# Kernel tuning notes

Measured on AMD Instinct MI355X. Metric: run time of the kernel, lower is better.

## Reference

```python
import jax, jax.numpy as jnp
import numpy as np

DIM = 192
HID = 128
EPS = 1e-8
ITERS = 3
LN_EPS = 1e-5
SCALE = DIM ** (-0.5)


def layer_norm(x, w, b):
    mu = x.mean(axis=-1, keepdims=True)
    var = ((x - mu) ** 2).mean(axis=-1, keepdims=True)
    return (x - mu) * jax.lax.rsqrt(var + LN_EPS) * w + b


def gru_cell(x, h, Wih, Whh, bih, bhh):
    # PyTorch GRUCell: gates ordered (r, z, n)
    gx = x @ Wih.T + bih          # [M, 3*DIM]
    gh = h @ Whh.T + bhh          # [M, 3*DIM]
    xr, xz, xn = jnp.split(gx, 3, axis=-1)
    hr, hz, hn = jnp.split(gh, 3, axis=-1)
    r = jax.nn.sigmoid(xr + hr)
    z = jax.nn.sigmoid(xz + hz)
    n = jnp.tanh(xn + r * hn)
    return (1.0 - z) * n + z * h


def setup_inputs() -> dict:
    key = jax.random.key(0)
    ks = jax.random.split(key, 12)
    B, N, K = 64, 4096, 11
    s = 0.02
    return {
        "inputs": jax.random.normal(ks[0], (B, N, DIM), jnp.float32),
        "noise": jax.random.normal(ks[1], (B, K, DIM), jnp.float32),
        "slots_mu": jax.random.normal(ks[2], (1, 1, DIM), jnp.float32),
        "slots_sigma": jax.random.uniform(ks[3], (1, 1, DIM), jnp.float32),
        "ln_in_w": jnp.ones((DIM,), jnp.float32),
        "ln_in_b": jnp.zeros((DIM,), jnp.float32),
        "ln_slots_w": jnp.ones((DIM,), jnp.float32),
        "ln_slots_b": jnp.zeros((DIM,), jnp.float32),
        "ln_mlp_w": jnp.ones((DIM,), jnp.float32),
        "ln_mlp_b": jnp.zeros((DIM,), jnp.float32),
        "Wq": jax.random.normal(ks[4], (DIM, DIM), jnp.float32) * s,
        "bq": jnp.zeros((DIM,), jnp.float32),
        "Wk": jax.random.normal(ks[5], (DIM, DIM), jnp.float32) * s,
        "bk": jnp.zeros((DIM,), jnp.float32),
        "Wv": jax.random.normal(ks[6], (DIM, DIM), jnp.float32) * s,
        "bv": jnp.zeros((DIM,), jnp.float32),
        "gru_Wih": jax.random.normal(ks[7], (3 * DIM, DIM), jnp.float32) * s,
        "gru_Whh": jax.random.normal(ks[8], (3 * DIM, DIM), jnp.float32) * s,
        "gru_bih": jnp.zeros((3 * DIM,), jnp.float32),
        "gru_bhh": jnp.zeros((3 * DIM,), jnp.float32),
        "mlp_W1": jax.random.normal(ks[9], (DIM, HID), jnp.float32) * s,
        "mlp_b1": jnp.zeros((HID,), jnp.float32),
        "mlp_W2": jax.random.normal(ks[10], (HID, DIM), jnp.float32) * s,
        "mlp_b2": jnp.zeros((DIM,), jnp.float32),
        "n_slots": 11,
    }


def reference(inputs, noise, slots_mu, slots_sigma,
              ln_in_w, ln_in_b, ln_slots_w, ln_slots_b, ln_mlp_w, ln_mlp_b,
              Wq, bq, Wk, bk, Wv, bv,
              gru_Wih, gru_Whh, gru_bih, gru_bhh,
              mlp_W1, mlp_b1, mlp_W2, mlp_b2, n_slots):
    B, N, _ = inputs.shape
    # slots ~ Normal(mu, sigma), reparameterized with fixed noise
    slots = slots_mu + slots_sigma * noise            # [B, K, D]
    x = layer_norm(inputs, ln_in_w, ln_in_b)
    key_vec = x @ Wk + bk                             # [B, N, D]
    val_vec = x @ Wv + bv                             # [B, N, D]
    attn_output = None
    for _ in range(ITERS):
        slots_prev = slots
        s_n = layer_norm(slots, ln_slots_w, ln_slots_b)
        q = s_n @ Wq + bq                             # [B, K, D]
        dots = jnp.einsum('bkd,bnd->bkn', q, key_vec) * SCALE
        attn = jax.nn.softmax(dots, axis=1) + EPS     # softmax over slots axis
        attn_output = attn
        attn = attn / attn.sum(axis=-1, keepdims=True)
        updates = jnp.einsum('bnd,bkn->bkd', val_vec, attn)
        h = gru_cell(updates.reshape(-1, DIM), slots_prev.reshape(-1, DIM),
                     gru_Wih, gru_Whh, gru_bih, gru_bhh)
        slots = h.reshape(B, -1, DIM)
        m = layer_norm(slots, ln_mlp_w, ln_mlp_b)
        m = jax.nn.relu(m @ mlp_W1 + mlp_b1) @ mlp_W2 + mlp_b2
        slots = slots + m
    return (slots, attn_output)
```

## Files before the change

kernel.cpp:

```cpp
#include <hip/hip_runtime.h>
#include <hip/hip_bf16.h>
#include <cstdint>
#include <cstddef>

#define DIM 192
#define NSL 11
#define NB 64
#define NN 4096
#define HIDN 128
#define NCHP 16
#define TROWS 32
#define NT 8
#define LN_EPS 1e-5f
#define EPS_A 1e-8f
#define SCALE_Q 0.07216878364870323f

__device__ __forceinline__ float wred(float v) {
#pragma unroll
  for (int m = 32; m; m >>= 1) v += __shfl_xor(v, m, 64);
  return v;
}

typedef const __attribute__((address_space(1))) void gas_void;
typedef __attribute__((address_space(3))) void las_void;
__device__ __forceinline__ void gload_lds16(const void* g, void* l) {
  __builtin_amdgcn_global_load_lds((gas_void*)g, (las_void*)l, 16, 0, 0);
}

__global__ __launch_bounds__(256) void k_tr(
    const float* __restrict__ Wih, const float* __restrict__ Whh, const float* __restrict__ Wk,
    float* __restrict__ WihT, float* __restrict__ WhhT, float* __restrict__ WkT) {
  __shared__ float t[64][65];
  int tile = blockIdx.x;
  const float* src; float* dst; int R, C;
  if (tile < 27)      { src = Wih; dst = WihT; R = 576; C = 192; }
  else if (tile < 54) { src = Whh; dst = WhhT; R = 576; C = 192; tile -= 27; }
  else                { src = Wk;  dst = WkT;  R = 192; C = 192; tile -= 54; }
  const int ntc = C >> 6;
  const int tr = tile / ntc, tc = tile % ntc;
  const int lane = threadIdx.x & 63, w = threadIdx.x >> 6;
#pragma unroll
  for (int i = 0; i < 16; ++i) {
    int row = w * 16 + i;
    t[row][lane] = src[(size_t)(tr * 64 + row) * C + tc * 64 + lane];
  }
  __syncthreads();
#pragma unroll
  for (int i = 0; i < 16; ++i) {
    int row = w * 16 + i;
    dst[(size_t)(tc * 64 + row) * R + tr * 64 + lane] = t[lane][row];
  }
}

__global__ __launch_bounds__(192) void k_prep(
    const float* __restrict__ lnw, const float* __restrict__ lnb,
    const float* __restrict__ Wq, const float* __restrict__ bq,
    const float* __restrict__ WkT, const float* __restrict__ bk,
    const float* __restrict__ xw, const float* __restrict__ xb,
    const float* __restrict__ noise, const float* __restrict__ mu0, const float* __restrict__ sig,
    float* __restrict__ slots_ws,
    float* __restrict__ qt, float* __restrict__ t0g, float* __restrict__ cpg) {
  const int b = blockIdx.x, kg = blockIdx.y, tid = threadIdx.x;
  const int k0 = kg * 3, kcnt = (kg == 3) ? 2 : 3;
  const int wave = tid >> 6, lane = tid & 63;
  const int j = tid;
  __shared__ __align__(16) float sn[3][DIM];
  __shared__ __align__(16) float qb[3][DIM];
  __shared__ float red[3][3][2];

#pragma unroll
  for (int kk = 0; kk < 3; ++kk) {
    if (kk < kcnt) {
      float v = mu0[j] + sig[j] * noise[(size_t)(b * NSL + k0 + kk) * DIM + j];
      sn[kk][j] = v;
      slots_ws[(size_t)(b * NSL + k0 + kk) * DIM + j] = v;
    } else sn[kk][j] = 0.f;
  }
  __syncthreads();

  for (int kk = wave; kk < 3; kk += 3) {
    float a = sn[kk][lane], c = sn[kk][lane + 64], e = sn[kk][lane + 128];
    float s = wred(a + c + e), ss = wred(a * a + c * c + e * e);
    float mu = s * (1.0f / DIM), var = ss * (1.0f / DIM) - mu * mu;
    float rstd = rsqrtf(var + LN_EPS);
    sn[kk][lane]       = (a - mu) * rstd * lnw[lane]       + lnb[lane];
    sn[kk][lane + 64]  = (c - mu) * rstd * lnw[lane + 64]  + lnb[lane + 64];
    sn[kk][lane + 128] = (e - mu) * rstd * lnw[lane + 128] + lnb[lane + 128];
  }
  __syncthreads();

  float acc[3];
  const float bj = bq[j];
#pragma unroll
  for (int kk = 0; kk < 3; ++kk) acc[kk] = bj;
  for (int d = 0; d < DIM; d += 4) {
    float w0 = Wq[(d + 0) * DIM + j], w1 = Wq[(d + 1) * DIM + j];
    float w2 = Wq[(d + 2) * DIM + j], w3 = Wq[(d + 3) * DIM + j];
#pragma unroll
    for (int kk = 0; kk < 3; ++kk) {
      float4 s4 = *(const float4*)&sn[kk][d];
      acc[kk] = fmaf(s4.w, w3, fmaf(s4.z, w2, fmaf(s4.y, w1, fmaf(s4.x, w0, acc[kk]))));
    }
  }
#pragma unroll
  for (int kk = 0; kk < 3; ++kk) qb[kk][j] = acc[kk];
  __syncthreads();

  float qk[3];
#pragma unroll
  for (int kk = 0; kk < 3; ++kk) qk[kk] = 0.f;
  for (int d = 0; d < DIM; d += 4) {
    float w0 = WkT[(d + 0) * DIM + j], w1 = WkT[(d + 1) * DIM + j];
    float w2 = WkT[(d + 2) * DIM + j], w3 = WkT[(d + 3) * DIM + j];
#pragma unroll
    for (int kk = 0; kk < 3; ++kk) {
      float4 q4 = *(const float4*)&qb[kk][d];
      qk[kk] = fmaf(q4.w, w3, fmaf(q4.z, w2, fmaf(q4.y, w1, fmaf(q4.x, w0, qk[kk]))));
    }
  }
  const float wj = xw[j], bxj = xb[j], bkj = bk[j];
#pragma unroll
  for (int kk = 0; kk < 3; ++kk) {
    float qtv = SCALE_Q * wj * qk[kk];
    if (kk < kcnt) qt[(size_t)(b * NSL + k0 + kk) * DIM + j] = qtv;
    float r1 = wred(qtv);
    float r2 = wred(SCALE_Q * (bxj * qk[kk] + qb[kk][j] * bkj));
    if (lane == 0) { red[wave][kk][0] = r1; red[wave][kk][1] = r2; }
  }
  __syncthreads();
  if (tid < kcnt) {
    t0g[b * NSL + k0 + tid] = red[0][tid][0] + red[1][tid][0] + red[2][tid][0];
    cpg[b * NSL + k0 + tid] = red[0][tid][1] + red[1][tid][1] + red[2][tid][1];
  }
}

__global__ __launch_bounds__(256) void k_iter(
    const float* __restrict__ x, const float* __restrict__ qt,
    const float* __restrict__ t0g, const float* __restrict__ cpg,
    float* __restrict__ attn_out, float* __restrict__ P1p,
    float* __restrict__ S_p, float* __restrict__ m1_p) {
  __shared__ __align__(16) float xs[2][TROWS * DIM];
  __shared__ __align__(16) float qs[NSL * DIM];
  __shared__ __align__(16) float a_lds[TROWS][12];
  __shared__ float rs_lds[TROWS];
  __shared__ float t0s[NSL], cps[NSL];
  __shared__ float redS[4][NSL], redM[4][NSL];

  const int b = blockIdx.x, ch = blockIdx.y, tid = threadIdx.x;
  const int lane = tid & 63, wv = tid >> 6;
  const int widx = tid & 15, g = tid >> 4;

  const float* xbase = x + ((size_t)b * NN + ch * 256) * DIM;

  {
#pragma unroll
    for (int i = 0; i < 6; ++i) {
      int c = i * 4 + wv;
      gload_lds16(xbase + c * 256 + lane * 4, &xs[0][c * 256]);
    }
  }
  {
    const float4* src = (const float4*)(qt + (size_t)b * NSL * DIM);
    float4* dst = (float4*)qs;
    dst[tid] = src[tid];
    dst[256 + tid] = src[256 + tid];
    if (tid < 16) dst[512 + tid] = src[512 + tid];
  }
  if (tid < NSL) { t0s[tid] = t0g[b * NSL + tid]; cps[tid] = cpg[b * NSL + tid]; }

  float acc[3][NSL], sS[NSL], sM[NSL];
#pragma unroll
  for (int k = 0; k < NSL; ++k) {
    acc[0][k] = 0.f; acc[1][k] = 0.f; acc[2][k] = 0.f;
    sS[k] = 0.f; sM[k] = 0.f;
  }

#pragma unroll 1
  for (int T = 0; T < NT; ++T) {
    const int cur = T & 1;
    __syncthreads();
    if (T < NT - 1) {
      const float* src = xbase + (size_t)(T + 1) * TROWS * DIM;
      float* dstb = &xs[cur ^ 1][0];
#pragma unroll
      for (int i = 0; i < 6; ++i) {
        int c = i * 4 + wv;
        gload_lds16(src + c * 256 + lane * 4, dstb + c * 256);
      }
      asm volatile("s_waitcnt vmcnt(6)" ::: "memory");
    } else {
      asm volatile("s_waitcnt vmcnt(0)" ::: "memory");
    }
    __builtin_amdgcn_s_barrier();
    const float* xc = &xs[cur][0];

    float dot[2][NSL], st_s[2], st_ss[2];
#pragma unroll
    for (int rr = 0; rr < 2; ++rr) {
      st_s[rr] = 0.f; st_ss[rr] = 0.f;
#pragma unroll
      for (int k = 0; k < NSL; ++k) dot[rr][k] = 0.f;
    }
#pragma unroll
    for (int w = 0; w < 3; ++w) {
      const int c4 = widx + 16 * w;
      float4 xr[2];
#pragma unroll
      for (int rr = 0; rr < 2; ++rr) {
        xr[rr] = ((const float4*)xc)[(2 * g + rr) * 48 + c4];
        st_s[rr] += (xr[rr].x + xr[rr].y) + (xr[rr].z + xr[rr].w);
        st_ss[rr] = fmaf(xr[rr].x, xr[rr].x, fmaf(xr[rr].y, xr[rr].y,
                    fmaf(xr[rr].z, xr[rr].z, fmaf(xr[rr].w, xr[rr].w, st_ss[rr]))));
      }
#pragma unroll
      for (int k = 0; k < NSL; ++k) {
        float4 qv = *(const float4*)&qs[k * DIM + 4 * c4];
#pragma unroll
        for (int rr = 0; rr < 2; ++rr)
          dot[rr][k] = fmaf(xr[rr].w, qv.w, fmaf(xr[rr].z, qv.z,
                       fmaf(xr[rr].y, qv.y, fmaf(xr[rr].x, qv.x, dot[rr][k]))));
      }
    }
#pragma unroll
    for (int m = 1; m <= 8; m <<= 1) {
#pragma unroll
      for (int rr = 0; rr < 2; ++rr) {
        st_s[rr] += __shfl_xor(st_s[rr], m, 64);
        st_ss[rr] += __shfl_xor(st_ss[rr], m, 64);
#pragma unroll
        for (int k = 0; k < NSL; ++k) dot[rr][k] += __shfl_xor(dot[rr][k], m, 64);
      }
    }
    if ((widx & 7) == 0) {
      const int hi = widx >> 3;
      const int r = 2 * g + hi;
      float dsel[NSL];
#pragma unroll
      for (int k = 0; k < NSL; ++k) dsel[k] = (widx == 0) ? dot[0][k] : dot[1][k];
      float sts  = (widx == 0) ? st_s[0]  : st_s[1];
      float stss = (widx == 0) ? st_ss[0] : st_ss[1];
      float mu = sts * (1.0f / DIM);
      float var = stss * (1.0f / DIM) - mu * mu;
      float rstd = rsqrtf(var + LN_EPS);
      float murstd = mu * rstd;
      float dv[NSL];
#pragma unroll
      for (int k = 0; k < NSL; ++k) dv[k] = fmaf(rstd, dsel[k], fmaf(-murstd, t0s[k], cps[k]));
      float mx = dv[0];
#pragma unroll
      for (int k = 1; k < NSL; ++k) mx = fmaxf(mx, dv[k]);
      float es[NSL], sum = 0.f;
#pragma unroll
      for (int k = 0; k < NSL; ++k) { es[k] = __expf(dv[k] - mx); sum += es[k]; }
      float inv = 1.0f / sum;
#pragma unroll
      for (int k = 0; k < NSL; ++k) {
        float a = fmaf(es[k], inv, EPS_A);
        a_lds[r][k] = a;
        sS[k] += a;
        sM[k] = fmaf(a, murstd, sM[k]);
      }
      rs_lds[r] = rstd;
    }
    asm volatile("s_waitcnt lgkmcnt(0)" ::: "memory");
    __builtin_amdgcn_s_barrier();

    {
      int idx = tid;
      attn_out[((size_t)(b * NSL + (idx >> 5))) * NN + ch * 256 + T * TROWS + (idx & 31)]
          = a_lds[idx & 31][idx >> 5];
      idx = tid + 256;
      if (idx < NSL * TROWS)
        attn_out[((size_t)(b * NSL + (idx >> 5))) * NN + ch * 256 + T * TROWS + (idx & 31)]
            = a_lds[idx & 31][idx >> 5];
    }
#pragma unroll 4
    for (int i = 0; i < 8; ++i) {
      const int r = 4 * i + wv;
      float rst = rs_lds[r];
      float4 a0 = *(const float4*)&a_lds[r][0];
      float4 a1 = *(const float4*)&a_lds[r][4];
      float4 a2 = *(const float4*)&a_lds[r][8];
#pragma unroll
      for (int j = 0; j < 3; ++j) {
        const int col = lane + 64 * j;
        float t1 = rst * xc[r * DIM + col];
        acc[j][0]  = fmaf(a0.x, t1, acc[j][0]);
        acc[j][1]  = fmaf(a0.y, t1, acc[j][1]);
        acc[j][2]  = fmaf(a0.z, t1, acc[j][2]);
        acc[j][3]  = fmaf(a0.w, t1, acc[j][3]);
        acc[j][4]  = fmaf(a1.x, t1, acc[j][4]);
        acc[j][5]  = fmaf(a1.y, t1, acc[j][5]);
        acc[j][6]  = fmaf(a1.z, t1, acc[j][6]);
        acc[j][7]  = fmaf(a1.w, t1, acc[j][7]);
        acc[j][8]  = fmaf(a2.x, t1, acc[j][8]);
        acc[j][9]  = fmaf(a2.y, t1, acc[j][9]);
        acc[j][10] = fmaf(a2.z, t1, acc[j][10]);
      }
    }
  }

  __syncthreads();
  float* accbuf = &xs[0][0];
#pragma unroll
  for (int j = 0; j < 3; ++j)
#pragma unroll
    for (int k = 0; k < NSL; ++k)
      accbuf[tid * 33 + j * 11 + k] = acc[j][k];
  __syncthreads();
  if (tid < DIM) {
    const int l = tid & 63, j = tid >> 6;
#pragma unroll
    for (int k = 0; k < NSL; ++k) {
      float v = accbuf[(l) * 33 + j * 11 + k] + accbuf[(64 + l) * 33 + j * 11 + k]
              + accbuf[(128 + l) * 33 + j * 11 + k] + accbuf[(192 + l) * 33 + j * 11 + k];
      P1p[(((size_t)b * NCHP + ch) * NSL + k) * DIM + tid] = v;
    }
  }
#pragma unroll
  for (int k = 0; k < NSL; ++k) { sS[k] = wred(sS[k]); sM[k] = wred(sM[k]); }
  if (lane == 0) {
#pragma unroll
    for (int k = 0; k < NSL; ++k) { redS[wv][k] = sS[k]; redM[wv][k] = sM[k]; }
  }
  __syncthreads();
  if (tid < NSL) {
    S_p[((size_t)b * NCHP + ch) * NSL + tid]  = redS[0][tid] + redS[1][tid] + redS[2][tid] + redS[3][tid];
    m1_p[((size_t)b * NCHP + ch) * NSL + tid] = redM[0][tid] + redM[1][tid] + redM[2][tid] + redM[3][tid];
  }
}

__global__ __launch_bounds__(192) void k_step(
    const float* __restrict__ P1p, const float* __restrict__ m1_p, const float* __restrict__ S_p,
    const float* __restrict__ xw, const float* __restrict__ xb,
    const float* __restrict__ Wv, const float* __restrict__ bv,
    const float* __restrict__ slots_in,
    const float* __restrict__ WihT, const float* __restrict__ WhhT,
    const float* __restrict__ bih, const float* __restrict__ bhh,
    const float* __restrict__ mw, const float* __restrict__ mb,
    const float* __restrict__ W1, const float* __restrict__ b1,
    const float* __restrict__ W2, const float* __restrict__ b2,
    const float* __restrict__ sw, const float* __restrict__ sb,
    const float* __restrict__ Wq, const float* __restrict__ bq,
    const float* __restrict__ WkT, const float* __restrict__ bk,
    float* __restrict__ slots_ws, float* __restrict__ slots_out,
    float* __restrict__ qt, float* __restrict__ t0g, float* __restrict__ cpg) {
  const int b = blockIdx.x, kg = blockIdx.y, tid = threadIdx.x;
  const int k0 = kg * 3, kcnt = (kg == 3) ? 2 : 3;
  const int wave = tid >> 6, lane = tid & 63;
  const int j = tid;
  __shared__ __align__(16) float u[3][DIM];
  __shared__ __align__(16) float hp[3][DIM];
  __shared__ __align__(16) float h[3][DIM];
  __shared__ __align__(16) float hid[3][HIDN];
  __shared__ float red[3][3][2];

  const float wj = xw[j], bj = xb[j];
#pragma unroll
  for (int kk = 0; kk < 3; ++kk) {
    if (kk < kcnt) {
      float p = 0.f, S = 0.f, M = 0.f;
#pragma unroll
      for (int ch = 0; ch < NCHP; ++ch) {
        p += P1p[(((size_t)b * NCHP + ch) * NSL + k0 + kk) * DIM + j];
        S += S_p[((size_t)b * NCHP + ch) * NSL + k0 + kk];
        M += m1_p[((size_t)b * NCHP + ch) * NSL + k0 + kk];
      }
      float inv = 1.0f / S;
      u[kk][j]  = wj * (p - M) * inv + bj;
      hp[kk][j] = slots_in[(size_t)(b * NSL + k0 + kk) * DIM + j];
    } else { u[kk][j] = 0.f; hp[kk][j] = 0.f; }
  }
  __syncthreads();

  float upd[3];
  const float bvj = bv[j];
#pragma unroll
  for (int kk = 0; kk < 3; ++kk) upd[kk] = bvj;
  for (int d = 0; d < DIM; d += 4) {
    float w0 = Wv[(d + 0) * DIM + j], w1 = Wv[(d + 1) * DIM + j];
    float w2 = Wv[(d + 2) * DIM + j], w3 = Wv[(d + 3) * DIM + j];
#pragma unroll
    for (int kk = 0; kk < 3; ++kk) {
      float4 x4 = *(const float4*)&u[kk][d];
      upd[kk] = fmaf(x4.w, w3, fmaf(x4.z, w2, fmaf(x4.y, w1, fmaf(x4.x, w0, upd[kk]))));
    }
  }
  __syncthreads();
#pragma unroll
  for (int kk = 0; kk < 3; ++kk) u[kk][j] = upd[kk];
  __syncthreads();

  float xr[3], xz[3], xn[3], hr[3], hz[3], hn[3];
  {
    float br_ = bih[j], bz_ = bih[DIM + j], bn_ = bih[2 * DIM + j];
    float cr_ = bhh[j], cz_ = bhh[DIM + j], cn_ = bhh[2 * DIM + j];
#pragma unroll
    for (int kk = 0; kk < 3; ++kk) { xr[kk] = br_; xz[kk] = bz_; xn[kk] = bn_; hr[kk] = cr_; hz[kk] = cz_; hn[kk] = cn_; }
  }
  for (int d = 0; d < DIM; d += 2) {
#pragma unroll
    for (int dd = 0; dd < 2; ++dd) {
      const float* ihrow = WihT + (size_t)(d + dd) * 576;
      const float* hhrow = WhhT + (size_t)(d + dd) * 576;
      float ar = ihrow[j], az = ihrow[192 + j], an = ihrow[384 + j];
      float br = hhrow[j], bz = hhrow[192 + j], bn = hhrow[384 + j];
#pragma unroll
      for (int kk = 0; kk < 3; ++kk) {
        float uv = u[kk][d + dd];
        float pv = hp[kk][d + dd];
        xr[kk] = fmaf(uv, ar, xr[kk]);
        xz[kk] = fmaf(uv, az, xz[kk]);
        xn[kk] = fmaf(uv, an, xn[kk]);
        hr[kk] = fmaf(pv, br, hr[kk]);
        hz[kk] = fmaf(pv, bz, hz[kk]);
        hn[kk] = fmaf(pv, bn, hn[kk]);
      }
    }
  }
#pragma unroll
  for (int kk = 0; kk < 3; ++kk) {
    float r = 1.f / (1.f + __expf(-(xr[kk] + hr[kk])));
    float z = 1.f / (1.f + __expf(-(xz[kk] + hz[kk])));
    float n = tanhf(xn[kk] + r * hn[kk]);
    h[kk][j] = (1.f - z) * n + z * hp[kk][j];
  }
  __syncthreads();

  for (int kk = wave; kk < 3; kk += 3) {
    float a = h[kk][lane], c = h[kk][lane + 64], e = h[kk][lane + 128];
    float s = wred(a + c + e), ss = wred(a * a + c * c + e * e);
    float mu = s * (1.0f / DIM), var = ss * (1.0f / DIM) - mu * mu;
    float rstd = rsqrtf(var + LN_EPS);
    u[kk][lane]       = (a - mu) * rstd * mw[lane]       + mb[lane];
    u[kk][lane + 64]  = (c - mu) * rstd * mw[lane + 64]  + mb[lane + 64];
    u[kk][lane + 128] = (e - mu) * rstd * mw[lane + 128] + mb[lane + 128];
  }
  __syncthreads();

  for (int t = tid; t < kcnt * HIDN; t += 192) {
    int kk = t >> 7, c = t & (HIDN - 1);
    float acc = b1[c];
    for (int d = 0; d < DIM; d += 4) {
      float4 m4 = *(const float4*)&u[kk][d];
      acc = fmaf(m4.x, W1[(d + 0) * HIDN + c],
            fmaf(m4.y, W1[(d + 1) * HIDN + c],
            fmaf(m4.z, W1[(d + 2) * HIDN + c],
            fmaf(m4.w, W1[(d + 3) * HIDN + c], acc))));
    }
    hid[kk][c] = fmaxf(acc, 0.f);
  }
  __syncthreads();

#pragma unroll 1
  for (int kk = 0; kk < kcnt; ++kk) {
    float acc = b2[j];
    for (int c = 0; c < HIDN; c += 4) {
      float4 h4 = *(const float4*)&hid[kk][c];
      acc = fmaf(h4.x, W2[(c + 0) * DIM + j],
            fmaf(h4.y, W2[(c + 1) * DIM + j],
            fmaf(h4.z, W2[(c + 2) * DIM + j],
            fmaf(h4.w, W2[(c + 3) * DIM + j], acc))));
    }
    float outv = h[kk][j] + acc;
    size_t gi = (size_t)(b * NSL + k0 + kk) * DIM + j;
    slots_ws[gi] = outv;
    slots_out[gi] = outv;
    hp[kk][j] = outv;
  }
  __syncthreads();

  for (int kk = wave; kk < 3; kk += 3) {
    float a = hp[kk][lane], c = hp[kk][lane + 64], e = hp[kk][lane + 128];
    float s = wred(a + c + e), ss = wred(a * a + c * c + e * e);
    float mu = s * (1.0f / DIM), var = ss * (1.0f / DIM) - mu * mu;
    float rstd = rsqrtf(var + LN_EPS);
    u[kk][lane]       = (a - mu) * rstd * sw[lane]       + sb[lane];
    u[kk][lane + 64]  = (c - mu) * rstd * sw[lane + 64]  + sb[lane + 64];
    u[kk][lane + 128] = (e - mu) * rstd * sw[lane + 128] + sb[lane + 128];
  }
  __syncthreads();

  float qacc[3];
  const float bqj = bq[j];
#pragma unroll
  for (int kk = 0; kk < 3; ++kk) qacc[kk] = bqj;
  for (int d = 0; d < DIM; d += 4) {
    float w0 = Wq[(d + 0) * DIM + j], w1 = Wq[(d + 1) * DIM + j];
    float w2 = Wq[(d + 2) * DIM + j], w3 = Wq[(d + 3) * DIM + j];
#pragma unroll
    for (int kk = 0; kk < 3; ++kk) {
      float4 s4 = *(const float4*)&u[kk][d];
      qacc[kk] = fmaf(s4.w, w3, fmaf(s4.z, w2, fmaf(s4.y, w1, fmaf(s4.x, w0, qacc[kk]))));
    }
  }
  __syncthreads();
#pragma unroll
  for (int kk = 0; kk < 3; ++kk) h[kk][j] = qacc[kk];
  __syncthreads();

  float qk[3];
#pragma unroll
  for (int kk = 0; kk < 3; ++kk) qk[kk] = 0.f;
  for (int d = 0; d < DIM; d += 4) {
    float w0 = WkT[(d + 0) * DIM + j], w1 = WkT[(d + 1) * DIM + j];
    float w2 = WkT[(d + 2) * DIM + j], w3 = WkT[(d + 3) * DIM + j];
#pragma unroll
    for (int kk = 0; kk < 3; ++kk) {
      float4 q4 = *(const float4*)&h[kk][d];
      qk[kk] = fmaf(q4.w, w3, fmaf(q4.z, w2, fmaf(q4.y, w1, fmaf(q4.x, w0, qk[kk]))));
    }
  }
  const float wxj = xw[j], bxj = xb[j], bkj = bk[j];
#pragma unroll
  for (int kk = 0; kk < 3; ++kk) {
    float qtv = SCALE_Q * wxj * qk[kk];
    if (kk < kcnt) qt[(size_t)(b * NSL + k0 + kk) * DIM + j] = qtv;
    float r1 = wred(qtv);
    float r2 = wred(SCALE_Q * (bxj * qk[kk] + h[kk][j] * bkj));
    if (lane == 0) { red[wave][kk][0] = r1; red[wave][kk][1] = r2; }
  }
  __syncthreads();
  if (tid < kcnt) {
    t0g[b * NSL + k0 + tid] = red[0][tid][0] + red[1][tid][0] + red[2][tid][0];
    cpg[b * NSL + k0 + tid] = red[0][tid][1] + red[1][tid][1] + red[2][tid][1];
  }
}

extern "C" void kernel_launch(void* const* d_in, const int* in_sizes, int n_in,
                              void* d_out, int out_size, void* d_ws, size_t ws_size,
                              hipStream_t stream) {
  const float* inputs      = (const float*)d_in[0];
  const float* noise       = (const float*)d_in[1];
  const float* slots_mu    = (const float*)d_in[2];
  const float* slots_sigma = (const float*)d_in[3];
  const float* ln_in_w     = (const float*)d_in[4];
  const float* ln_in_b     = (const float*)d_in[5];
  const float* ln_slots_w  = (const float*)d_in[6];
  const float* ln_slots_b  = (const float*)d_in[7];
  const float* ln_mlp_w    = (const float*)d_in[8];
  const float* ln_mlp_b    = (const float*)d_in[9];
  const float* Wq  = (const float*)d_in[10];
  const float* bq  = (const float*)d_in[11];
  const float* Wk  = (const float*)d_in[12];
  const float* bk  = (const float*)d_in[13];
  const float* Wv  = (const float*)d_in[14];
  const float* bv  = (const float*)d_in[15];
  const float* Wih = (const float*)d_in[16];
  const float* Whh = (const float*)d_in[17];
  const float* bih = (const float*)d_in[18];
  const float* bhh = (const float*)d_in[19];
  const float* W1  = (const float*)d_in[20];
  const float* b1  = (const float*)d_in[21];
  const float* W2  = (const float*)d_in[22];
  const float* b2  = (const float*)d_in[23];

  float* out = (float*)d_out;
  float* slots_out = out;
  float* attn_out  = out + NB * NSL * DIM;

  char* w = (char*)d_ws;
  float* slots = (float*)w;
  float* qt    = (float*)(w + 540672);
  float* t0g   = (float*)(w + 1081344);
  float* cpg   = (float*)(w + 1084160);
  float* P1p   = (float*)(w + 1086976);
  float* S_p   = (float*)(w + 9737728);
  float* m1_p  = (float*)(w + 9782784);
  float* WihT  = (float*)(w + 9827840);
  float* WhhT  = (float*)(w + 10270208);
  float* WkT   = (float*)(w + 10712576);

  k_tr<<<63, 256, 0, stream>>>(Wih, Whh, Wk, WihT, WhhT, WkT);
  k_prep<<<dim3(NB, 4), 192, 0, stream>>>(ln_slots_w, ln_slots_b, Wq, bq, WkT, bk,
                                          ln_in_w, ln_in_b, noise, slots_mu, slots_sigma,
                                          slots, qt, t0g, cpg);
  for (int it = 0; it < 3; ++it) {
    k_iter<<<dim3(NB, NCHP), 256, 0, stream>>>(inputs, qt, t0g, cpg, attn_out, P1p, S_p, m1_p);
    k_step<<<dim3(NB, 4), 192, 0, stream>>>(P1p, m1_p, S_p, ln_in_w, ln_in_b, Wv, bv, slots,
                                            WihT, WhhT, bih, bhh, ln_mlp_w, ln_mlp_b,
                                            W1, b1, W2, b2, ln_slots_w, ln_slots_b,
                                            Wq, bq, WkT, bk, slots, slots_out, qt, t0g, cpg);
  }
}
```

Measured before the change: 771.8 us.

## Single-buffer x tile in k_iter for occupancy; one slot per k_step block

k_iter drops its double-buffered LDS tile for a single buffer and requests 4 blocks per CU through launch bounds, so each tile load is now waited on before compute. The cross-wave accumulator reduction is done in two passes so it fits in the smaller buffer. k_step now handles one slot per block (grid NB x 11) instead of three, giving more blocks with fewer registers each. The aim is higher occupancy and parallelism, at the cost of losing load/compute overlap within a block and re-reading weights per slot.

```diff
diff --git a/kernel.cpp b/kernel.cpp
--- a/kernel.cpp
+++ b/kernel.cpp
@@ -134,12 +134,12 @@
   }
 }
 
-__global__ __launch_bounds__(256) void k_iter(
+__global__ __launch_bounds__(256, 4) void k_iter(
     const float* __restrict__ x, const float* __restrict__ qt,
     const float* __restrict__ t0g, const float* __restrict__ cpg,
     float* __restrict__ attn_out, float* __restrict__ P1p,
     float* __restrict__ S_p, float* __restrict__ m1_p) {
-  __shared__ __align__(16) float xs[2][TROWS * DIM];
+  __shared__ __align__(16) float xs[TROWS * DIM];
   __shared__ __align__(16) float qs[NSL * DIM];
   __shared__ __align__(16) float a_lds[TROWS][12];
   __shared__ float rs_lds[TROWS];
@@ -152,12 +152,10 @@
 
   const float* xbase = x + ((size_t)b * NN + ch * 256) * DIM;
 
-  {
-#pragma unroll
-    for (int i = 0; i < 6; ++i) {
-      int c = i * 4 + wv;
-      gload_lds16(xbase + c * 256 + lane * 4, &xs[0][c * 256]);
-    }
+#pragma unroll
+  for (int i = 0; i < 6; ++i) {
+    int c = i * 4 + wv;
+    gload_lds16(xbase + c * 256 + lane * 4, &xs[c * 256]);
   }
   {
     const float4* src = (const float4*)(qt + (size_t)b * NSL * DIM);
@@ -177,22 +175,19 @@
 
 #pragma unroll 1
   for (int T = 0; T < NT; ++T) {
-    const int cur = T & 1;
-    __syncthreads();
-    if (T < NT - 1) {
-      const float* src = xbase + (size_t)(T + 1) * TROWS * DIM;
-      float* dstb = &xs[cur ^ 1][0];
+    if (T == 0) {
+      __syncthreads();
+    } else {
+      __syncthreads();
+      const float* src = xbase + (size_t)T * TROWS * DIM;
 #pragma unroll
       for (int i = 0; i < 6; ++i) {
         int c = i * 4 + wv;
-        gload_lds16(src + c * 256 + lane * 4, dstb + c * 256);
+        gload_lds16(src + c * 256 + lane * 4, &xs[c * 256]);
       }
-      asm volatile("s_waitcnt vmcnt(6)" ::: "memory");
-    } else {
       asm volatile("s_waitcnt vmcnt(0)" ::: "memory");
-    }
-    __builtin_amdgcn_s_barrier();
-    const float* xc = &xs[cur][0];
+      __builtin_amdgcn_s_barrier();
+    }
 
     float dot[2][NSL], st_s[2], st_ss[2];
 #pragma unroll
@@ -207,7 +202,7 @@
       float4 xr[2];
 #pragma unroll
       for (int rr = 0; rr < 2; ++rr) {
-        xr[rr] = ((const float4*)xc)[(2 * g + rr) * 48 + c4];
+        xr[rr] = ((const float4*)xs)[(2 * g + rr) * 48 + c4];
         st_s[rr] += (xr[rr].x + xr[rr].y) + (xr[rr].z + xr[rr].w);
         st_ss[rr] = fmaf(xr[rr].x, xr[rr].x, fmaf(xr[rr].y, xr[rr].y,
                     fmaf(xr[rr].z, xr[rr].z, fmaf(xr[rr].w, xr[rr].w, st_ss[rr]))));
@@ -284,7 +279,7 @@
 #pragma unroll
       for (int j = 0; j < 3; ++j) {
         const int col = lane + 64 * j;
-        float t1 = rst * xc[r * DIM + col];
+        float t1 = rst * xs[r * DIM + col];
         acc[j][0]  = fmaf(a0.x, t1, acc[j][0]);
         acc[j][1]  = fmaf(a0.y, t1, acc[j][1]);
         acc[j][2]  = fmaf(a0.z, t1, acc[j][2]);
@@ -301,19 +296,29 @@
   }
 
   __syncthreads();
-  float* accbuf = &xs[0][0];
-#pragma unroll
-  for (int j = 0; j < 3; ++j)
-#pragma unroll
-    for (int k = 0; k < NSL; ++k)
-      accbuf[tid * 33 + j * 11 + k] = acc[j][k];
+  float* accbuf = &xs[0];
+  const int slot = tid & 127;
+  if (wv < 2) {
+#pragma unroll
+    for (int j = 0; j < 3; ++j)
+#pragma unroll
+      for (int k = 0; k < NSL; ++k)
+        accbuf[slot * 33 + j * 11 + k] = acc[j][k];
+  }
+  __syncthreads();
+  if (wv >= 2) {
+#pragma unroll
+    for (int j = 0; j < 3; ++j)
+#pragma unroll
+      for (int k = 0; k < NSL; ++k)
+        accbuf[slot * 33 + j * 11 + k] += acc[j][k];
+  }
   __syncthreads();
   if (tid < DIM) {
     const int l = tid & 63, j = tid >> 6;
 #pragma unroll
     for (int k = 0; k < NSL; ++k) {
-      float v = accbuf[(l) * 33 + j * 11 + k] + accbuf[(64 + l) * 33 + j * 11 + k]
-              + accbuf[(128 + l) * 33 + j * 11 + k] + accbuf[(192 + l) * 33 + j * 11 + k];
+      float v = accbuf[l * 33 + j * 11 + k] + accbuf[(64 + l) * 33 + j * 11 + k];
       P1p[(((size_t)b * NCHP + ch) * NSL + k) * DIM + tid] = v;
     }
   }
@@ -345,185 +350,160 @@
     const float* __restrict__ WkT, const float* __restrict__ bk,
     float* __restrict__ slots_ws, float* __restrict__ slots_out,
     float* __restrict__ qt, float* __restrict__ t0g, float* __restrict__ cpg) {
-  const int b = blockIdx.x, kg = blockIdx.y, tid = threadIdx.x;
-  const int k0 = kg * 3, kcnt = (kg == 3) ? 2 : 3;
+  const int b = blockIdx.x, k = blockIdx.y, tid = threadIdx.x;
   const int wave = tid >> 6, lane = tid & 63;
   const int j = tid;
-  __shared__ __align__(16) float u[3][DIM];
-  __shared__ __align__(16) float hp[3][DIM];
-  __shared__ __align__(16) float h[3][DIM];
-  __shared__ __align__(16) float hid[3][HIDN];
-  __shared__ float red[3][3][2];
-
-  const float wj = xw[j], bj = xb[j];
-#pragma unroll
-  for (int kk = 0; kk < 3; ++kk) {
-    if (kk < kcnt) {
-      float p = 0.f, S = 0.f, M = 0.f;
-#pragma unroll
-      for (int ch = 0; ch < NCHP; ++ch) {
-        p += P1p[(((size_t)b * NCHP + ch) * NSL + k0 + kk) * DIM + j];
-        S += S_p[((size_t)b * NCHP + ch) * NSL + k0 + kk];
-        M += m1_p[((size_t)b * NCHP + ch) * NSL + k0 + kk];
-      }
-      float inv = 1.0f / S;
-      u[kk][j]  = wj * (p - M) * inv + bj;
-      hp[kk][j] = slots_in[(size_t)(b * NSL + k0 + kk) * DIM + j];
-    } else { u[kk][j] = 0.f; hp[kk][j] = 0.f; }
-  }
-  __syncthreads();
-
-  float upd[3];
-  const float bvj = bv[j];
-#pragma unroll
-  for (int kk = 0; kk < 3; ++kk) upd[kk] = bvj;
+  __shared__ __align__(16) float u[DIM];
+  __shared__ __align__(16) float hp[DIM];
+  __shared__ __align__(16) float h[DIM];
+  __shared__ __align__(16) float hid[HIDN];
+  __shared__ float red[3][2];
+
+  {
+    float p = 0.f, S = 0.f, M = 0.f;
+#pragma unroll
+    for (int ch = 0; ch < NCHP; ++ch) {
+      p += P1p[(((size_t)b * NCHP + ch) * NSL + k) * DIM + j];
+      S += S_p[((size_t)b * NCHP + ch) * NSL + k];
+      M += m1_p[((size_t)b * NCHP + ch) * NSL + k];
+    }
+    float inv = 1.0f / S;
+    u[j]  = xw[j] * (p - M) * inv + xb[j];
+    hp[j] = slots_in[(size_t)(b * NSL + k) * DIM + j];
+  }
+  __syncthreads();
+
+  float upd = bv[j];
+#pragma unroll 2
   for (int d = 0; d < DIM; d += 4) {
-    float w0 = Wv[(d + 0) * DIM + j], w1 = Wv[(d + 1) * DIM + j];
-    float w2 = Wv[(d + 2) * DIM + j], w3 = Wv[(d + 3) * DIM + j];
-#pragma unroll
-    for (int kk = 0; kk < 3; ++kk) {
-      float4 x4 = *(const float4*)&u[kk][d];
-      upd[kk] = fmaf(x4.w, w3, fmaf(x4.z, w2, fmaf(x4.y, w1, fmaf(x4.x, w0, upd[kk]))));
-    }
-  }
-  __syncthreads();
-#pragma unroll
-  for (int kk = 0; kk < 3; ++kk) u[kk][j] = upd[kk];
-  __syncthreads();
-
-  float xr[3], xz[3], xn[3], hr[3], hz[3], hn[3];
-  {
-    float br_ = bih[j], bz_ = bih[DIM + j], bn_ = bih[2 * DIM + j];
-    float cr_ = bhh[j], cz_ = bhh[DIM + j], cn_ = bhh[2 * DIM + j];
-#pragma unroll
-    for (int kk = 0; kk < 3; ++kk) { xr[kk] = br_; xz[kk] = bz_; xn[kk] = bn_; hr[kk] = cr_; hz[kk] = cz_; hn[kk] = cn_; }
-  }
-  for (int d = 0; d < DIM; d += 2) {
-#pragma unroll
-    for (int dd = 0; dd < 2; ++dd) {
+    float4 u4 = *(const float4*)&u[d];
+    upd = fmaf(u4.x, Wv[(d + 0) * DIM + j],
+          fmaf(u4.y, Wv[(d + 1) * DIM + j],
+          fmaf(u4.z, Wv[(d + 2) * DIM + j],
+          fmaf(u4.w, Wv[(d + 3) * DIM + j], upd))));
+  }
+  __syncthreads();
+  u[j] = upd;
+  __syncthreads();
+
+  float xr = bih[j], xz = bih[DIM + j], xn = bih[2 * DIM + j];
+  float hr = bhh[j], hz = bhh[DIM + j], hn = bhh[2 * DIM + j];
+#pragma unroll 2
+  for (int d = 0; d < DIM; d += 4) {
+    float4 u4 = *(const float4*)&u[d];
+    float4 p4 = *(const float4*)&hp[d];
+    float us[4] = {u4.x, u4.y, u4.z, u4.w};
+    float ps[4] = {p4.x, p4.y, p4.z, p4.w};
+#pragma unroll
+    for (int dd = 0; dd < 4; ++dd) {
       const float* ihrow = WihT + (size_t)(d + dd) * 576;
       const float* hhrow = WhhT + (size_t)(d + dd) * 576;
-      float ar = ihrow[j], az = ihrow[192 + j], an = ihrow[384 + j];
-      float br = hhrow[j], bz = hhrow[192 + j], bn = hhrow[384 + j];
-#pragma unroll
-      for (int kk = 0; kk < 3; ++kk) {
-        float uv = u[kk][d + dd];
-        float pv = hp[kk][d + dd];
-        xr[kk] = fmaf(uv, ar, xr[kk]);
-        xz[kk] = fmaf(uv, az, xz[kk]);
-        xn[kk] = fmaf(uv, an, xn[kk]);
-        hr[kk] = fmaf(pv, br, hr[kk]);
-        hz[kk] = fmaf(pv, bz, hz[kk]);
-        hn[kk] = fmaf(pv, bn, hn[kk]);
-      }
-    }
-  }
-#pragma unroll
-  for (int kk = 0; kk < 3; ++kk) {
-    float r = 1.f / (1.f + __expf(-(xr[kk] + hr[kk])));
-    float z = 1.f / (1.f + __expf(-(xz[kk] + hz[kk])));
-    float n = tanhf(xn[kk] + r * hn[kk]);
-    h[kk][j] = (1.f - z) * n + z * hp[kk][j];
-  }
-  __syncthreads();
-
-  for (int kk = wave; kk < 3; kk += 3) {
-    float a = h[kk][lane], c = h[kk][lane + 64], e = h[kk][lane + 128];
+      xr = fmaf(us[dd], ihrow[j], xr);
+      xz = fmaf(us[dd], ihrow[192 + j], xz);
+      xn = fmaf(us[dd], ihrow[384 + j], xn);
+      hr = fmaf(ps[dd], hhrow[j], hr);
+      hz = fmaf(ps[dd], hhrow[192 + j], hz);
+      hn = fmaf(ps[dd], hhrow[384 + j], hn);
+    }
+  }
+  float hv;
+  {
+    float r = 1.f / (1.f + __expf(-(xr + hr)));
+    float z = 1.f / (1.f + __expf(-(xz + hz)));
+    float n = tanhf(xn + r * hn);
+    hv = (1.f - z) * n + z * hp[j];
+    h[j] = hv;
+  }
+  __syncthreads();
+
+  {
+    float a = h[lane], c = h[lane + 64], e = h[lane + 128];
     float s = wred(a + c + e), ss = wred(a * a + c * c + e * e);
     float mu = s * (1.0f / DIM), var = ss * (1.0f / DIM) - mu * mu;
     float rstd = rsqrtf(var + LN_EPS);
-    u[kk][lane]       = (a - mu) * rstd * mw[lane]       + mb[lane];
-    u[kk][lane + 64]  = (c - mu) * rstd * mw[lane + 64]  + mb[lane + 64];
-    u[kk][lane + 128] = (e - mu) * rstd * mw[lane + 128] + mb[lane + 128];
-  }
-  __syncthreads();
-
-  for (int t = tid; t < kcnt * HIDN; t += 192) {
-    int kk = t >> 7, c = t & (HIDN - 1);
-    float acc = b1[c];
+    u[lane]       = (a - mu) * rstd * mw[lane]       + mb[lane];
+    u[lane + 64]  = (c - mu) * rstd * mw[lane + 64]  + mb[lane + 64];
+    u[lane + 128] = (e - mu) * rstd * mw[lane + 128] + mb[lane + 128];
+  }
+  __syncthreads();
+
+  if (tid < HIDN) {
+    float acc = b1[tid];
+#pragma unroll 2
     for (int d = 0; d < DIM; d += 4) {
-      float4 m4 = *(const float4*)&u[kk][d];
-      acc = fmaf(m4.x, W1[(d + 0) * HIDN + c],
-            fmaf(m4.y, W1[(d + 1) * HIDN + c],
-            fmaf(m4.z, W1[(d + 2) * HIDN + c],
-            fmaf(m4.w, W1[(d + 3) * HIDN + c], acc))));
-    }
-    hid[kk][c] = fmaxf(acc, 0.f);
-  }
-  __syncthreads();
-
-#pragma unroll 1
-  for (int kk = 0; kk < kcnt; ++kk) {
+      float4 m4 = *(const float4*)&u[d];
+      acc = fmaf(m4.x, W1[(d + 0) * HIDN + tid],
+            fmaf(m4.y, W1[(d + 1) * HIDN + tid],
+            fmaf(m4.z, W1[(d + 2) * HIDN + tid],
+            fmaf(m4.w, W1[(d + 3) * HIDN + tid], acc))));
+    }
+    hid[tid] = fmaxf(acc, 0.f);
+  }
+  __syncthreads();
+
+  float outv;
+  {
     float acc = b2[j];
+#pragma unroll 2
     for (int c = 0; c < HIDN; c += 4) {
-      float4 h4 = *(const float4*)&hid[kk][c];
+      float4 h4 = *(const float4*)&hid[c];
       acc = fmaf(h4.x, W2[(c + 0) * DIM + j],
             fmaf(h4.y, W2[(c + 1) * DIM + j],
             fmaf(h4.z, W2[(c + 2) * DIM + j],
             fmaf(h4.w, W2[(c + 3) * DIM + j], acc))));
     }
-    float outv = h[kk][j] + acc;
-    size_t gi = (size_t)(b * NSL + k0 + kk) * DIM + j;
+    outv = hv + acc;
+    size_t gi = (size_t)(b * NSL + k) * DIM + j;
     slots_ws[gi] = outv;
     slots_out[gi] = outv;
-    hp[kk][j] = outv;
-  }
-  __syncthreads();
-
-  for (int kk = wave; kk < 3; kk += 3) {
-    float a = hp[kk][lane], c = hp[kk][lane + 64], e = hp[kk][lane + 128];
+    hp[j] = outv;
+  }
+  __syncthreads();
+
+  {
+    float a = hp[lane], c = hp[lane + 64], e = hp[lane + 128];
     float s = wred(a + c + e), ss = wred(a * a + c * c + e * e);
     float mu = s * (1.0f / DIM), var = ss * (1.0f / DIM) - mu * mu;
     float rstd = rsqrtf(var + LN_EPS);
-    u[kk][lane]       = (a - mu) * rstd * sw[lane]       + sb[lane];
-    u[kk][lane + 64]  = (c - mu) * rstd * sw[lane + 64]  + sb[lane + 64];
-    u[kk][lane + 128] = (e - mu) * rstd * sw[lane + 128] + sb[lane + 128];
-  }
-  __syncthreads();
-
-  float qacc[3];
-  const float bqj = bq[j];
-#pragma unroll
-  for (int kk = 0; kk < 3; ++kk) qacc[kk] = bqj;
+    u[lane]       = (a - mu) * rstd * sw[lane]       + sb[lane];
+    u[lane + 64]  = (c - mu) * rstd * sw[lane + 64]  + sb[lane + 64];
+    u[lane + 128] = (e - mu) * rstd * sw[lane + 128] + sb[lane + 128];
+  }
+  __syncthreads();
+
+  float qacc = bq[j];
+#pragma unroll 2
   for (int d = 0; d < DIM; d += 4) {
-    float w0 = Wq[(d + 0) * DIM + j], w1 = Wq[(d + 1) * DIM + j];
-    float w2 = Wq[(d + 2) * DIM + j], w3 = Wq[(d + 3) * DIM + j];
-#pragma unroll
-    for (int kk = 0; kk < 3; ++kk) {
-      float4 s4 = *(const float4*)&u[kk][d];
-      qacc[kk] = fmaf(s4.w, w3, fmaf(s4.z, w2, fmaf(s4.y, w1, fmaf(s4.x, w0, qacc[kk]))));
-    }
-  }
-  __syncthreads();
-#pragma unroll
-  for (int kk = 0; kk < 3; ++kk) h[kk][j] = qacc[kk];
-  __syncthreads();
-
-  float qk[3];
-#pragma unroll
-  for (int kk = 0; kk < 3; ++kk) qk[kk] = 0.f;
+    float4 s4 = *(const float4*)&u[d];
+    qacc = fmaf(s4.x, Wq[(d + 0) * DIM + j],
+           fmaf(s4.y, Wq[(d + 1) * DIM + j],
+           fmaf(s4.z, Wq[(d + 2) * DIM + j],
+           fmaf(s4.w, Wq[(d + 3) * DIM + j], qacc))));
+  }
+  __syncthreads();
+  h[j] = qacc;
+  __syncthreads();
+
+  float qk = 0.f;
+#pragma unroll 2
   for (int d = 0; d < DIM; d += 4) {
-    float w0 = WkT[(d + 0) * DIM + j], w1 = WkT[(d + 1) * DIM + j];
-    float w2 = WkT[(d + 2) * DIM + j], w3 = WkT[(d + 3) * DIM + j];
-#pragma unroll
-    for (int kk = 0; kk < 3; ++kk) {
-      float4 q4 = *(const float4*)&h[kk][d];
-      qk[kk] = fmaf(q4.w, w3, fmaf(q4.z, w2, fmaf(q4.y, w1, fmaf(q4.x, w0, qk[kk]))));
-    }
-  }
-  const float wxj = xw[j], bxj = xb[j], bkj = bk[j];
-#pragma unroll
-  for (int kk = 0; kk < 3; ++kk) {
-    float qtv = SCALE_Q * wxj * qk[kk];
-    if (kk < kcnt) qt[(size_t)(b * NSL + k0 + kk) * DIM + j] = qtv;
+    float4 q4 = *(const float4*)&h[d];
+    qk = fmaf(q4.x, WkT[(d + 0) * DIM + j],
+         fmaf(q4.y, WkT[(d + 1) * DIM + j],
+         fmaf(q4.z, WkT[(d + 2) * DIM + j],
+         fmaf(q4.w, WkT[(d + 3) * DIM + j], qk))));
+  }
+  {
+    float qtv = SCALE_Q * xw[j] * qk;
+    qt[(size_t)(b * NSL + k) * DIM + j] = qtv;
     float r1 = wred(qtv);
-    float r2 = wred(SCALE_Q * (bxj * qk[kk] + h[kk][j] * bkj));
-    if (lane == 0) { red[wave][kk][0] = r1; red[wave][kk][1] = r2; }
-  }
-  __syncthreads();
-  if (tid < kcnt) {
-    t0g[b * NSL + k0 + tid] = red[0][tid][0] + red[1][tid][0] + red[2][tid][0];
-    cpg[b * NSL + k0 + tid] = red[0][tid][1] + red[1][tid][1] + red[2][tid][1];
+    float r2 = wred(SCALE_Q * (xb[j] * qk + qacc * bk[j]));
+    if (lane == 0) { red[wave][0] = r1; red[wave][1] = r2; }
+  }
+  __syncthreads();
+  if (tid == 0) {
+    t0g[b * NSL + k] = red[0][0] + red[1][0] + red[2][0];
+    cpg[b * NSL + k] = red[0][1] + red[1][1] + red[2][1];
   }
 }
 
@@ -577,9 +557,9 @@
                                           slots, qt, t0g, cpg);
   for (int it = 0; it < 3; ++it) {
     k_iter<<<dim3(NB, NCHP), 256, 0, stream>>>(inputs, qt, t0g, cpg, attn_out, P1p, S_p, m1_p);
-    k_step<<<dim3(NB, 4), 192, 0, stream>>>(P1p, m1_p, S_p, ln_in_w, ln_in_b, Wv, bv, slots,
-                                            WihT, WhhT, bih, bhh, ln_mlp_w, ln_mlp_b,
-                                            W1, b1, W2, b2, ln_slots_w, ln_slots_b,
-                                            Wq, bq, WkT, bk, slots, slots_out, qt, t0g, cpg);
-  }
-}
+    k_step<<<dim3(NB, NSL), 192, 0, stream>>>(P1p, m1_p, S_p, ln_in_w, ln_in_b, Wv, bv, slots,
+                                              WihT, WhhT, bih, bhh, ln_mlp_w, ln_mlp_b,
+                                              W1, b1, W2, b2, ln_slots_w, ln_slots_b,
+                                              Wq, bq, WkT, bk, slots, slots_out, qt, t0g, cpg);
+  }
+}
```

Result: no change. 760.0 us (-1.5%).
